# Kernel optimization log

Measured on AMD Instinct MI355X. Metric: run time of the kernel, lower is better.

The kernel has to match this reference:

```python
import jax, jax.numpy as jnp
import numpy as np

D_MODEL = 2048
N_HEAD = 16
D_K = D_MODEL // N_HEAD  # 128
B, S = 2, 2048


def setup_inputs() -> dict:
    key = jax.random.key(0)
    ks = jax.random.split(key, 10)
    std = 1.0 / np.sqrt(D_MODEL)
    inp = {
        "x": jax.random.normal(ks[0], (B, S, D_MODEL), dtype=jnp.float32),
        "mask": jnp.ones((B, 1, S, S), dtype=jnp.int32),
        # Linear weights stored as [in, out] for x @ W + b
        "w_q": jax.random.normal(ks[1], (D_MODEL, D_MODEL), dtype=jnp.float32) * std,
        "b_q": jnp.zeros((D_MODEL,), dtype=jnp.float32),
        "w_k": jax.random.normal(ks[2], (D_MODEL, D_K), dtype=jnp.float32) * std,
        "b_k": jnp.zeros((D_K,), dtype=jnp.float32),
        "w_v": jax.random.normal(ks[3], (D_MODEL, D_K), dtype=jnp.float32) * std,
        "b_v": jnp.zeros((D_K,), dtype=jnp.float32),
        "w_o": jax.random.normal(ks[4], (D_MODEL, D_MODEL), dtype=jnp.float32) * std,
        "b_o": jnp.zeros((D_MODEL,), dtype=jnp.float32),
    }
    return inp


def reference(x, mask, w_q, b_q, w_k, b_k, w_v, b_v, w_o, b_o):
    b, s, _ = x.shape
    # Q: [b, h, s, d_k]; K/V single shared head: [b, 1, s, d_k]
    q = (x @ w_q + b_q).reshape(b, s, N_HEAD, D_K).transpose(0, 2, 1, 3)
    k = (x @ w_k + b_k)[:, None, :, :]
    v = (x @ w_v + b_v)[:, None, :, :]
    scale = jnp.sqrt(jnp.float32(D_K))
    # scores: [b, h, s, s] (K head broadcast over h)
    scores = jnp.einsum("bhqd,bzkd->bhqk", q, k) / scale
    scores = jnp.where(mask == 0, jnp.float32(-jnp.inf), scores)
    attn = jax.nn.softmax(scores, axis=-1)
    out = jnp.einsum("bhqk,bzkd->bhqd", attn, v)  # [b, h, s, d_k]
    out = out.transpose(0, 2, 1, 3).reshape(b, s, D_MODEL)
    return out @ w_o + b_o
```

## Files before the change

### kernel.cpp

```cpp
#include <hip/hip_runtime.h>

typedef __attribute__((ext_vector_type(8))) short bf16x8;
typedef __attribute__((ext_vector_type(4))) float f32x4;

#define GLD_LDS16(g, l)                                                        \
  __builtin_amdgcn_global_load_lds(                                            \
      (const __attribute__((address_space(1))) void*)(g),                      \
      (__attribute__((address_space(3))) void*)(l), 16, 0, 0)

__device__ __forceinline__ f32x4 mfma_bf16(bf16x8 a, bf16x8 b, f32x4 c) {
  return __builtin_amdgcn_mfma_f32_16x16x32_bf16(a, b, c, 0, 0, 0);
}

__device__ __forceinline__ unsigned short f2bf(float f) {
  union { float f; unsigned int u; } a;
  a.f = f;
  unsigned int u = a.u;
  unsigned int r = (u + 0x7fffu + ((u >> 16) & 1u)) >> 16;
  return (unsigned short)r;
}


__global__ void k_convert(const float* __restrict__ in,
                          unsigned short* __restrict__ out, int n8) {
  int i = blockIdx.x * 256 + threadIdx.x;
  if (i >= n8) return;
  const float4* p = reinterpret_cast<const float4*>(in) + (size_t)i * 2;
  float4 a = p[0], b = p[1];
  union { unsigned short u[8]; uint4 v; } pk;
  pk.u[0] = f2bf(a.x); pk.u[1] = f2bf(a.y); pk.u[2] = f2bf(a.z); pk.u[3] = f2bf(a.w);
  pk.u[4] = f2bf(b.x); pk.u[5] = f2bf(b.y); pk.u[6] = f2bf(b.z); pk.u[7] = f2bf(b.w);
  reinterpret_cast<uint4*>(out)[i] = pk.v;
}

__global__ void k_transpose(const float* __restrict__ in,
                            unsigned short* __restrict__ out, int R, int C) {
  __shared__ float tile[32][33];
  int c0 = blockIdx.x * 32, r0 = blockIdx.y * 32;
  int tx = threadIdx.x, ty = threadIdx.y;
#pragma unroll
  for (int j = 0; j < 4; ++j)
    tile[ty + j * 8][tx] = in[(size_t)(r0 + ty + j * 8) * C + (c0 + tx)];
  __syncthreads();
#pragma unroll
  for (int j = 0; j < 4; ++j)
    out[(size_t)(c0 + ty + j * 8) * R + (r0 + tx)] = f2bf(tile[tx][ty + j * 8]);
}

__global__ void k_bias_concat(const float* __restrict__ bq,
                              const float* __restrict__ bk,
                              const float* __restrict__ bv,
                              float* __restrict__ o) {
  int i = blockIdx.x * 256 + threadIdx.x;
  if (i < 2048) o[i] = bq[i];
  else if (i < 2176) o[i] = bk[i - 2048];
  else if (i < 2304) o[i] = bv[i - 2176];
}


template <bool OUT_F32>
__global__ __launch_bounds__(256, 2) void k_gemm(
    const unsigned short* __restrict__ A, const unsigned short* __restrict__ Bt,
    const float* __restrict__ bias, void* __restrict__ Cp, int M, int N, int K) {
  __shared__ __align__(16) unsigned short lda[128 * 32];
  __shared__ __align__(16) unsigned short ldb[128 * 32];
  const int t = threadIdx.x;
  const int l = t & 63;
  const int w = t >> 6;
  const int wr = w >> 1, wc = w & 1;
  const int lr = l & 15, lg = l >> 4;
  const int m0 = blockIdx.y * 128, n0 = blockIdx.x * 128;

  f32x4 acc[4][4] = {};

  for (int kt = 0; kt < K; kt += 32) {
#pragma unroll
    for (int c = 0; c < 2; ++c) {
      int idx = t * 8 + c * 2048;
      int row = idx >> 5, col = idx & 31;
      GLD_LDS16(A + (size_t)(m0 + row) * K + kt + col, lda + w * 512 + c * 2048);
      GLD_LDS16(Bt + (size_t)(n0 + row) * K + kt + col, ldb + w * 512 + c * 2048);
    }
    __syncthreads();
    bf16x8 af[4], bfr[4];
#pragma unroll
    for (int i = 0; i < 4; ++i)
      af[i] = *reinterpret_cast<const bf16x8*>(lda + (wr * 64 + i * 16 + lr) * 32 + lg * 8);
#pragma unroll
    for (int j = 0; j < 4; ++j)
      bfr[j] = *reinterpret_cast<const bf16x8*>(ldb + (wc * 64 + j * 16 + lr) * 32 + lg * 8);
#pragma unroll
    for (int i = 0; i < 4; ++i)
#pragma unroll
      for (int j = 0; j < 4; ++j)
        acc[i][j] = mfma_bf16(af[i], bfr[j], acc[i][j]);
    __syncthreads();
  }

#pragma unroll
  for (int j = 0; j < 4; ++j) {
    int col = n0 + wc * 64 + j * 16 + lr;
    float bv = bias[col];
#pragma unroll
    for (int i = 0; i < 4; ++i) {
      int rowb = m0 + wr * 64 + i * 16 + lg * 4;
#pragma unroll
      for (int r = 0; r < 4; ++r) {
        float v = acc[i][j][r] + bv;
        if (OUT_F32)
          reinterpret_cast<float*>(Cp)[(size_t)(rowb + r) * N + col] = v;
        else
          reinterpret_cast<unsigned short*>(Cp)[(size_t)(rowb + r) * N + col] = f2bf(v);
      }
    }
  }
}


__global__ __launch_bounds__(256, 2) void k_attn(
    const unsigned short* __restrict__ qkv, unsigned short* __restrict__ out) {
  __shared__ __align__(16) unsigned short q_lds[128 * 128];
  __shared__ __align__(16) unsigned short k_lds[64 * 128];
  __shared__ __align__(16) unsigned short v_lds[128 * 72];
  unsigned short* p_lds = q_lds;

  const int t = threadIdx.x, l = t & 63, w = t >> 6;
  const int lr = l & 15, lg = l >> 4;
  const int bid = blockIdx.x;
  const int qt = bid & 15, h = (bid >> 4) & 15, b = bid >> 8;
  const size_t rowQ0 = (size_t)b * 2048 + qt * 128;
  const size_t rowK0 = (size_t)b * 2048;

#pragma unroll
  for (int c = 0; c < 8; ++c) {
    int f16 = t + c * 256;
    int row = f16 >> 4, col16 = f16 & 15;
    GLD_LDS16(qkv + (rowQ0 + row) * 2304 + h * 128 + col16 * 8,
              q_lds + w * 512 + c * 2048);
  }
  __syncthreads();

  bf16x8 qf[2][4];
#pragma unroll
  for (int rt = 0; rt < 2; ++rt)
#pragma unroll
    for (int kd = 0; kd < 4; ++kd)
      qf[rt][kd] = *reinterpret_cast<const bf16x8*>(
          q_lds + (w * 32 + rt * 16 + lr) * 128 + kd * 32 + lg * 8);

  f32x4 o_acc[2][8] = {};
  float m_s[2][4], l_s[2][4];
#pragma unroll
  for (int rt = 0; rt < 2; ++rt)
#pragma unroll
    for (int r = 0; r < 4; ++r) { m_s[rt][r] = -1e30f; l_s[rt][r] = 0.f; }

  const float C_SM = 0.08838834764831845f * 1.4426950408889634f;

  for (int kc = 0; kc < 32; ++kc) {
#pragma unroll
    for (int c = 0; c < 4; ++c) {
      int f16 = t + c * 256;
      int row = f16 >> 4;
      int col16 = (f16 & 15) ^ (row & 7);
      GLD_LDS16(qkv + (rowK0 + kc * 64 + row) * 2304 + 2048 + col16 * 8,
                k_lds + w * 512 + c * 2048);
    }
#pragma unroll
    for (int c = 0; c < 4; ++c) {
      int i = l;
      int d0 = w * 32 + c * 8;
      bf16x8 vv = *reinterpret_cast<const bf16x8*>(
          qkv + (rowK0 + kc * 64 + i) * 2304 + 2176 + d0);
#pragma unroll
      for (int e = 0; e < 8; ++e)
        v_lds[(d0 + e) * 72 + i] = (unsigned short)vv[e];
    }
    __syncthreads();

    f32x4 sf[2][4];
#pragma unroll
    for (int ctK = 0; ctK < 4; ++ctK) {
      f32x4 s0 = {0.f, 0.f, 0.f, 0.f}, s1 = {0.f, 0.f, 0.f, 0.f};
#pragma unroll
      for (int kd = 0; kd < 4; ++kd) {
        int row = ctK * 16 + lr;
        int u = (kd * 4 + lg) ^ (row & 7);
        bf16x8 kf = *reinterpret_cast<const bf16x8*>(k_lds + row * 128 + u * 8);
        s0 = mfma_bf16(qf[0][kd], kf, s0);
        s1 = mfma_bf16(qf[1][kd], kf, s1);
      }
      sf[0][ctK] = s0; sf[1][ctK] = s1;
    }

#pragma unroll
    for (int rt = 0; rt < 2; ++rt) {
#pragma unroll
      for (int r = 0; r < 4; ++r) {
        float v = fmaxf(fmaxf(sf[rt][0][r], sf[rt][1][r]),
                        fmaxf(sf[rt][2][r], sf[rt][3][r]));
        v = fmaxf(v, __shfl_xor(v, 1));
        v = fmaxf(v, __shfl_xor(v, 2));
        v = fmaxf(v, __shfl_xor(v, 4));
        v = fmaxf(v, __shfl_xor(v, 8));
        float newm = fmaxf(m_s[rt][r], v);
        float alpha = __builtin_amdgcn_exp2f((m_s[rt][r] - newm) * C_SM);
        m_s[rt][r] = newm;
        float psum = 0.f;
#pragma unroll
        for (int ctK = 0; ctK < 4; ++ctK) {
          float p = __builtin_amdgcn_exp2f((sf[rt][ctK][r] - newm) * C_SM);
          sf[rt][ctK][r] = p;
          psum += p;
        }
        psum += __shfl_xor(psum, 1);
        psum += __shfl_xor(psum, 2);
        psum += __shfl_xor(psum, 4);
        psum += __shfl_xor(psum, 8);
        l_s[rt][r] = l_s[rt][r] * alpha + psum;
#pragma unroll
        for (int ct8 = 0; ct8 < 8; ++ct8) o_acc[rt][ct8][r] *= alpha;
      }
#pragma unroll
      for (int ctK = 0; ctK < 4; ++ctK)
#pragma unroll
        for (int r = 0; r < 4; ++r)
          p_lds[(w * 32 + rt * 16 + lg * 4 + r) * 72 + ctK * 16 + lr] =
              f2bf(sf[rt][ctK][r]);
    }

#pragma unroll
    for (int ks = 0; ks < 2; ++ks) {
      bf16x8 pf[2];
#pragma unroll
      for (int rt = 0; rt < 2; ++rt)
        pf[rt] = *reinterpret_cast<const bf16x8*>(
            p_lds + (w * 32 + rt * 16 + lr) * 72 + ks * 32 + lg * 8);
#pragma unroll
      for (int ct8 = 0; ct8 < 8; ++ct8) {
        bf16x8 vf = *reinterpret_cast<const bf16x8*>(
            v_lds + (ct8 * 16 + lr) * 72 + ks * 32 + lg * 8);
        o_acc[0][ct8] = mfma_bf16(pf[0], vf, o_acc[0][ct8]);
        o_acc[1][ct8] = mfma_bf16(pf[1], vf, o_acc[1][ct8]);
      }
    }
    __syncthreads();
  }

#pragma unroll
  for (int rt = 0; rt < 2; ++rt) {
    float inv[4];
#pragma unroll
    for (int r = 0; r < 4; ++r) inv[r] = 1.0f / l_s[rt][r];
#pragma unroll
    for (int ct8 = 0; ct8 < 8; ++ct8) {
      int col = h * 128 + ct8 * 16 + lr;
#pragma unroll
      for (int r = 0; r < 4; ++r) {
        size_t row = rowQ0 + w * 32 + rt * 16 + lg * 4 + r;
        out[row * 2048 + col] = f2bf(o_acc[rt][ct8][r] * inv[r]);
      }
    }
  }
}


extern "C" void kernel_launch(void* const* d_in, const int* in_sizes, int n_in,
                              void* d_out, int out_size, void* d_ws,
                              size_t ws_size, hipStream_t stream) {
  const float* x  = (const float*)d_in[0];
  const float* wq = (const float*)d_in[2];
  const float* bq = (const float*)d_in[3];
  const float* wk = (const float*)d_in[4];
  const float* bk = (const float*)d_in[5];
  const float* wv = (const float*)d_in[6];
  const float* bv = (const float*)d_in[7];
  const float* wo = (const float*)d_in[8];
  const float* bo = (const float*)d_in[9];
  float* out = (float*)d_out;

  char* ws = (char*)d_ws;
  unsigned short* xb    = (unsigned short*)(ws);
  unsigned short* wqkvT = (unsigned short*)(ws + 16777216);
  unsigned short* woT   = (unsigned short*)(ws + 26214400);
  unsigned short* qkvb  = (unsigned short*)(ws + 34603008);
  float*          biasq = (float*)(ws + 53477376);

  k_convert<<<4096, 256, 0, stream>>>(x, xb, 1048576);
  k_transpose<<<dim3(64, 64), dim3(32, 8), 0, stream>>>(wq, wqkvT, 2048, 2048);
  k_transpose<<<dim3(4, 64),  dim3(32, 8), 0, stream>>>(wk, wqkvT + (size_t)2048 * 2048, 2048, 128);
  k_transpose<<<dim3(4, 64),  dim3(32, 8), 0, stream>>>(wv, wqkvT + (size_t)2176 * 2048, 2048, 128);
  k_transpose<<<dim3(64, 64), dim3(32, 8), 0, stream>>>(wo, woT, 2048, 2048);
  k_bias_concat<<<9, 256, 0, stream>>>(bq, bk, bv, biasq);

  k_gemm<false><<<dim3(18, 32), 256, 0, stream>>>(xb, wqkvT, biasq, qkvb, 4096, 2304, 2048);
  k_attn<<<512, 256, 0, stream>>>(qkvb, xb);
  k_gemm<true><<<dim3(16, 32), 256, 0, stream>>>(xb, woT, bo, out, 4096, 2048, 2048);
}
```

Before: 423.8 us.

## Restructure attention kernel to 8 waves with double-buffered K/V prefetch

Moves the attention kernel from 4 waves handling 32 query rows each to 8 waves handling 16 rows each. Q fragments now load straight into registers, and K is double-buffered in LDS, with the next tile prefetched asynchronously while the current one computes. V is prefetched into registers and then stored transposed with a new 68-element pitch. The online softmax also skips rescaling when the row max does not change. The costs are an extra barrier per iteration, more LDS per block, and possible bank conflicts from the new V pitch.

```diff
diff --git a/kernel.cpp b/kernel.cpp
--- a/kernel.cpp
+++ b/kernel.cpp
@@ -117,12 +117,11 @@
 }
 
 
-__global__ __launch_bounds__(256, 2) void k_attn(
+__global__ __launch_bounds__(512, 4) void k_attn(
     const unsigned short* __restrict__ qkv, unsigned short* __restrict__ out) {
-  __shared__ __align__(16) unsigned short q_lds[128 * 128];
-  __shared__ __align__(16) unsigned short k_lds[64 * 128];
-  __shared__ __align__(16) unsigned short v_lds[128 * 72];
-  unsigned short* p_lds = q_lds;
+  __shared__ __align__(16) unsigned short k_lds[2][64 * 128];
+  __shared__ __align__(16) unsigned short v_lds[128 * 68];
+  __shared__ __align__(16) unsigned short p_lds[128 * 72];
 
   const int t = threadIdx.x, l = t & 63, w = t >> 6;
   const int lr = l & 15, lg = l >> 4;
@@ -131,136 +130,139 @@
   const size_t rowQ0 = (size_t)b * 2048 + qt * 128;
   const size_t rowK0 = (size_t)b * 2048;
 
-#pragma unroll
-  for (int c = 0; c < 8; ++c) {
-    int f16 = t + c * 256;
-    int row = f16 >> 4, col16 = f16 & 15;
-    GLD_LDS16(qkv + (rowQ0 + row) * 2304 + h * 128 + col16 * 8,
-              q_lds + w * 512 + c * 2048);
-  }
+  bf16x8 qf[4];
+  {
+    const unsigned short* qrow = qkv + (rowQ0 + w * 16 + lr) * 2304 + h * 128;
+#pragma unroll
+    for (int kd = 0; kd < 4; ++kd)
+      qf[kd] = *reinterpret_cast<const bf16x8*>(qrow + kd * 32 + lg * 8);
+  }
+
+#pragma unroll
+  for (int c = 0; c < 2; ++c) {
+    int f16 = t + c * 512;
+    int row = f16 >> 4;
+    int col16 = (f16 & 15) ^ (row & 7);
+    GLD_LDS16(qkv + (rowK0 + row) * 2304 + 2048 + col16 * 8,
+              &k_lds[0][0] + w * 512 + c * 4096);
+  }
+  bf16x8 vst[2];
+#pragma unroll
+  for (int c = 0; c < 2; ++c)
+    vst[c] = *reinterpret_cast<const bf16x8*>(
+        qkv + (rowK0 + l) * 2304 + 2176 + w * 16 + c * 8);
+#pragma unroll
+  for (int c = 0; c < 2; ++c)
+#pragma unroll
+    for (int e = 0; e < 8; ++e)
+      v_lds[(w * 16 + c * 8 + e) * 68 + l] = (unsigned short)vst[c][e];
   __syncthreads();
 
-  bf16x8 qf[2][4];
-#pragma unroll
-  for (int rt = 0; rt < 2; ++rt)
-#pragma unroll
-    for (int kd = 0; kd < 4; ++kd)
-      qf[rt][kd] = *reinterpret_cast<const bf16x8*>(
-          q_lds + (w * 32 + rt * 16 + lr) * 128 + kd * 32 + lg * 8);
-
-  f32x4 o_acc[2][8] = {};
-  float m_s[2][4], l_s[2][4];
-#pragma unroll
-  for (int rt = 0; rt < 2; ++rt)
-#pragma unroll
-    for (int r = 0; r < 4; ++r) { m_s[rt][r] = -1e30f; l_s[rt][r] = 0.f; }
+  f32x4 o_acc[8] = {};
+  float m_s[4], l_s[4];
+#pragma unroll
+  for (int r = 0; r < 4; ++r) { m_s[r] = -1e30f; l_s[r] = 0.f; }
 
   const float C_SM = 0.08838834764831845f * 1.4426950408889634f;
 
   for (int kc = 0; kc < 32; ++kc) {
-#pragma unroll
-    for (int c = 0; c < 4; ++c) {
-      int f16 = t + c * 256;
-      int row = f16 >> 4;
-      int col16 = (f16 & 15) ^ (row & 7);
-      GLD_LDS16(qkv + (rowK0 + kc * 64 + row) * 2304 + 2048 + col16 * 8,
-                k_lds + w * 512 + c * 2048);
-    }
-#pragma unroll
-    for (int c = 0; c < 4; ++c) {
-      int i = l;
-      int d0 = w * 32 + c * 8;
-      bf16x8 vv = *reinterpret_cast<const bf16x8*>(
-          qkv + (rowK0 + kc * 64 + i) * 2304 + 2176 + d0);
-#pragma unroll
-      for (int e = 0; e < 8; ++e)
-        v_lds[(d0 + e) * 72 + i] = (unsigned short)vv[e];
-    }
-    __syncthreads();
-
-    f32x4 sf[2][4];
+    const int cur = kc & 1;
+    const unsigned short* kl = &k_lds[cur][0];
+
+    if (kc < 31) {
+#pragma unroll
+      for (int c = 0; c < 2; ++c) {
+        int f16 = t + c * 512;
+        int row = f16 >> 4;
+        int col16 = (f16 & 15) ^ (row & 7);
+        GLD_LDS16(qkv + (rowK0 + (kc + 1) * 64 + row) * 2304 + 2048 + col16 * 8,
+                  &k_lds[cur ^ 1][0] + w * 512 + c * 4096);
+      }
+#pragma unroll
+      for (int c = 0; c < 2; ++c)
+        vst[c] = *reinterpret_cast<const bf16x8*>(
+            qkv + (rowK0 + (kc + 1) * 64 + l) * 2304 + 2176 + w * 16 + c * 8);
+    }
+
+    f32x4 sf[4];
 #pragma unroll
     for (int ctK = 0; ctK < 4; ++ctK) {
-      f32x4 s0 = {0.f, 0.f, 0.f, 0.f}, s1 = {0.f, 0.f, 0.f, 0.f};
+      f32x4 s = {0.f, 0.f, 0.f, 0.f};
 #pragma unroll
       for (int kd = 0; kd < 4; ++kd) {
         int row = ctK * 16 + lr;
         int u = (kd * 4 + lg) ^ (row & 7);
-        bf16x8 kf = *reinterpret_cast<const bf16x8*>(k_lds + row * 128 + u * 8);
-        s0 = mfma_bf16(qf[0][kd], kf, s0);
-        s1 = mfma_bf16(qf[1][kd], kf, s1);
-      }
-      sf[0][ctK] = s0; sf[1][ctK] = s1;
-    }
-
-#pragma unroll
-    for (int rt = 0; rt < 2; ++rt) {
-#pragma unroll
-      for (int r = 0; r < 4; ++r) {
-        float v = fmaxf(fmaxf(sf[rt][0][r], sf[rt][1][r]),
-                        fmaxf(sf[rt][2][r], sf[rt][3][r]));
-        v = fmaxf(v, __shfl_xor(v, 1));
-        v = fmaxf(v, __shfl_xor(v, 2));
-        v = fmaxf(v, __shfl_xor(v, 4));
-        v = fmaxf(v, __shfl_xor(v, 8));
-        float newm = fmaxf(m_s[rt][r], v);
-        float alpha = __builtin_amdgcn_exp2f((m_s[rt][r] - newm) * C_SM);
-        m_s[rt][r] = newm;
-        float psum = 0.f;
-#pragma unroll
-        for (int ctK = 0; ctK < 4; ++ctK) {
-          float p = __builtin_amdgcn_exp2f((sf[rt][ctK][r] - newm) * C_SM);
-          sf[rt][ctK][r] = p;
-          psum += p;
-        }
-        psum += __shfl_xor(psum, 1);
-        psum += __shfl_xor(psum, 2);
-        psum += __shfl_xor(psum, 4);
-        psum += __shfl_xor(psum, 8);
-        l_s[rt][r] = l_s[rt][r] * alpha + psum;
-#pragma unroll
-        for (int ct8 = 0; ct8 < 8; ++ct8) o_acc[rt][ct8][r] *= alpha;
-      }
-#pragma unroll
-      for (int ctK = 0; ctK < 4; ++ctK)
-#pragma unroll
-        for (int r = 0; r < 4; ++r)
-          p_lds[(w * 32 + rt * 16 + lg * 4 + r) * 72 + ctK * 16 + lr] =
-              f2bf(sf[rt][ctK][r]);
-    }
+        bf16x8 kf = *reinterpret_cast<const bf16x8*>(kl + row * 128 + u * 8);
+        s = mfma_bf16(qf[kd], kf, s);
+      }
+      sf[ctK] = s;
+    }
+
+#pragma unroll
+    for (int r = 0; r < 4; ++r) {
+      float v = fmaxf(fmaxf(sf[0][r], sf[1][r]), fmaxf(sf[2][r], sf[3][r]));
+      v = fmaxf(v, __shfl_xor(v, 1));
+      v = fmaxf(v, __shfl_xor(v, 2));
+      v = fmaxf(v, __shfl_xor(v, 4));
+      v = fmaxf(v, __shfl_xor(v, 8));
+      if (!__all(v <= m_s[r])) {
+        float newm = fmaxf(m_s[r], v);
+        float alpha = __builtin_amdgcn_exp2f((m_s[r] - newm) * C_SM);
+        m_s[r] = newm;
+        l_s[r] *= alpha;
+#pragma unroll
+        for (int ct8 = 0; ct8 < 8; ++ct8) o_acc[ct8][r] *= alpha;
+      }
+      float psum = 0.f;
+#pragma unroll
+      for (int ctK = 0; ctK < 4; ++ctK) {
+        float p = __builtin_amdgcn_exp2f((sf[ctK][r] - m_s[r]) * C_SM);
+        sf[ctK][r] = p;
+        psum += p;
+      }
+      psum += __shfl_xor(psum, 1);
+      psum += __shfl_xor(psum, 2);
+      psum += __shfl_xor(psum, 4);
+      psum += __shfl_xor(psum, 8);
+      l_s[r] += psum;
+    }
+
+#pragma unroll
+    for (int ctK = 0; ctK < 4; ++ctK)
+#pragma unroll
+      for (int r = 0; r < 4; ++r)
+        p_lds[(w * 16 + lg * 4 + r) * 72 + ctK * 16 + lr] = f2bf(sf[ctK][r]);
 
 #pragma unroll
     for (int ks = 0; ks < 2; ++ks) {
-      bf16x8 pf[2];
-#pragma unroll
-      for (int rt = 0; rt < 2; ++rt)
-        pf[rt] = *reinterpret_cast<const bf16x8*>(
-            p_lds + (w * 32 + rt * 16 + lr) * 72 + ks * 32 + lg * 8);
+      bf16x8 pf = *reinterpret_cast<const bf16x8*>(
+          p_lds + (w * 16 + lr) * 72 + ks * 32 + lg * 8);
 #pragma unroll
       for (int ct8 = 0; ct8 < 8; ++ct8) {
         bf16x8 vf = *reinterpret_cast<const bf16x8*>(
-            v_lds + (ct8 * 16 + lr) * 72 + ks * 32 + lg * 8);
-        o_acc[0][ct8] = mfma_bf16(pf[0], vf, o_acc[0][ct8]);
-        o_acc[1][ct8] = mfma_bf16(pf[1], vf, o_acc[1][ct8]);
-      }
-    }
+            v_lds + (ct8 * 16 + lr) * 68 + ks * 32 + lg * 8);
+        o_acc[ct8] = mfma_bf16(pf, vf, o_acc[ct8]);
+      }
+    }
+
     __syncthreads();
-  }
-
-#pragma unroll
-  for (int rt = 0; rt < 2; ++rt) {
-    float inv[4];
-#pragma unroll
-    for (int r = 0; r < 4; ++r) inv[r] = 1.0f / l_s[rt][r];
-#pragma unroll
-    for (int ct8 = 0; ct8 < 8; ++ct8) {
-      int col = h * 128 + ct8 * 16 + lr;
-#pragma unroll
-      for (int r = 0; r < 4; ++r) {
-        size_t row = rowQ0 + w * 32 + rt * 16 + lg * 4 + r;
-        out[row * 2048 + col] = f2bf(o_acc[rt][ct8][r] * inv[r]);
-      }
-    }
+    if (kc < 31) {
+#pragma unroll
+      for (int c = 0; c < 2; ++c)
+#pragma unroll
+        for (int e = 0; e < 8; ++e)
+          v_lds[(w * 16 + c * 8 + e) * 68 + l] = (unsigned short)vst[c][e];
+    }
+    __syncthreads();
+  }
+
+#pragma unroll
+  for (int r = 0; r < 4; ++r) {
+    float inv = 1.0f / l_s[r];
+    size_t row = rowQ0 + w * 16 + lg * 4 + r;
+#pragma unroll
+    for (int ct8 = 0; ct8 < 8; ++ct8)
+      out[row * 2048 + h * 128 + ct8 * 16 + lr] = f2bf(o_acc[ct8][r] * inv);
   }
 }
 
@@ -294,6 +296,6 @@
   k_bias_concat<<<9, 256, 0, stream>>>(bq, bk, bv, biasq);
 
   k_gemm<false><<<dim3(18, 32), 256, 0, stream>>>(xb, wqkvT, biasq, qkvb, 4096, 2304, 2048);
-  k_attn<<<512, 256, 0, stream>>>(qkvb, xb);
+  k_attn<<<512, 512, 0, stream>>>(qkvb, xb);
   k_gemm<true><<<dim3(16, 32), 256, 0, stream>>>(xb, woT, bo, out, 4096, 2048, 2048);
 }
```

Measured after the change: 414.8 us. 1.02x faster.
